# Kernel optimization log

Measured on AMD Instinct MI355X. Metric: run time of the kernel, lower is better.

## Reference

```python
import jax, jax.numpy as jnp
import numpy as np

B, LC, LQ, D = 256, 400, 50, 128
NEG = 1e12


def setup_inputs() -> dict:
    key = jax.random.key(0)
    ks = jax.random.split(key, 7)
    return {
        "x_cont": jax.random.normal(ks[0], (B, LC, D), dtype=jnp.float32),
        "x_ques": jax.random.normal(ks[1], (B, LQ, D), dtype=jnp.float32),
        "W0": jax.random.normal(ks[2], (D, 1), dtype=jnp.float32) * (1.0 / np.sqrt(D)),
        "W1": jax.random.normal(ks[3], (D, 1), dtype=jnp.float32) * (1.0 / np.sqrt(D)),
        "W2": jax.random.normal(ks[4], (1, 1, D), dtype=jnp.float32) * (1.0 / np.sqrt(D)),
        "cont_len": jax.random.randint(ks[5], (B, 1), 1, LC, dtype=jnp.int32),
        "ques_len": jax.random.randint(ks[6], (B, 1), 1, LQ, dtype=jnp.int32),
    }


def reference(x_cont, x_ques, W0, W1, W2, cont_len, ques_len):
    # Trilinear similarity S[b,c,q] = xc.W0 + xq.W1 + (xc*W2).xq
    s_c = x_cont @ W0                                   # (B, LC, 1)
    s_q = jnp.swapaxes(x_ques @ W1, 1, 2)               # (B, 1, LQ)
    s_f = jnp.einsum('bcd,bqd->bcq', x_cont * W2, x_ques)
    S = s_c + s_q + s_f                                 # (B, LC, LQ)

    # Length masks: position valid iff pos < seq_len (matches one_hot+cumsum)
    q_mask = (jnp.arange(LQ)[None, :] < ques_len).astype(S.dtype)  # (B, LQ)
    c_mask = (jnp.arange(LC)[None, :] < cont_len).astype(S.dtype)  # (B, LC)

    S_bar = jax.nn.softmax(S - (1.0 - q_mask)[:, None, :] * NEG, axis=-1)
    S_T = jnp.swapaxes(
        jax.nn.softmax(S - (1.0 - c_mask)[:, :, None] * NEG, axis=1), 1, 2)  # (B, LQ, LC)

    c2q = S_bar @ x_ques                                # (B, LC, D)
    q2c = (S_bar @ S_T) @ x_cont                        # (B, LC, D)

    result = jnp.concatenate(
        [x_cont, c2q, x_cont * c2q, x_cont * q2c], axis=-1)  # (B, LC, 4D)
    return result, S_bar, S_T
```

## Files before the change

### kernel.cpp

```cpp
#include <hip/hip_runtime.h>
#include <math.h>

#define B 256
#define LC 400
#define LQ 50
#define D 128
#define CT 64

__global__ __launch_bounds__(256, 2) void k_scores_rowsm(
    const float* __restrict__ xc_g, const float* __restrict__ xq_g,
    const float* __restrict__ W0, const float* __restrict__ W1,
    const float* __restrict__ W2, const int* __restrict__ ques_len,
    float* __restrict__ S_bar, float* __restrict__ S_Traw)
{
    __shared__ __align__(16) float xq[56 * 132];
    __shared__ __align__(16) float xc[CT * 132];
    __shared__ float w[3 * D];
    __shared__ float sq[56], sc[CT];
    __shared__ float sS[CT * 51];
    __shared__ float rowm[CT], rowi[CT];

    const int b = blockIdx.y;
    const int c0 = blockIdx.x * CT;
    const int t = threadIdx.x;
    const int nc = min(CT, LC - c0);
    const int qlen = ques_len[b];

    const float4* xq4g = (const float4*)(xq_g + (size_t)b * LQ * D);
    for (int i = t; i < 56 * 32; i += 256) {
        float4 v = (i < LQ * 32) ? xq4g[i] : make_float4(0.f, 0.f, 0.f, 0.f);
        ((float4*)xq)[(i >> 5) * 33 + (i & 31)] = v;
    }
    const float4* xc4g = (const float4*)(xc_g + (size_t)(b * LC + c0) * D);
    for (int i = t; i < nc * 32; i += 256)
        ((float4*)xc)[(i >> 5) * 33 + (i & 31)] = xc4g[i];
    if (t < D) { w[t] = W0[t]; w[D + t] = W1[t]; w[2 * D + t] = W2[t]; }
    __syncthreads();

    if (t < LQ) {
        const float4* r = (const float4*)(xq + t * 132);
        const float4* wv = (const float4*)(w + D);
        float4 a = {0.f, 0.f, 0.f, 0.f};
#pragma unroll
        for (int d = 0; d < 32; ++d) {
            float4 u = r[d], v = wv[d];
            a.x += u.x * v.x; a.y += u.y * v.y; a.z += u.z * v.z; a.w += u.w * v.w;
        }
        sq[t] = a.x + a.y + a.z + a.w;
    } else if (t >= 64 && t < 128) {
        const int c = t - 64;
        if (c < nc) {
            const float4* r = (const float4*)(xc + c * 132);
            const float4* wv = (const float4*)w;
            float4 a = {0.f, 0.f, 0.f, 0.f};
#pragma unroll
            for (int d = 0; d < 32; ++d) {
                float4 u = r[d], v = wv[d];
                a.x += u.x * v.x; a.y += u.y * v.y; a.z += u.z * v.z; a.w += u.w * v.w;
            }
            sc[c] = a.x + a.y + a.z + a.w;
        }
    }
    __syncthreads();
    for (int i = t; i < LQ * D; i += 256)
        xq[(i >> 7) * 132 + (i & 127)] *= w[2 * D + (i & 127)];
    __syncthreads();

    const int qg = t & 7;
    const int cg = (t >> 3) & 15;
    const int half = t >> 7;
    const int d0 = half * 16;

    float acc[4][7];
#pragma unroll
    for (int k = 0; k < 4; ++k)
#pragma unroll
        for (int j = 0; j < 7; ++j) acc[k][j] = 0.f;

    {
        const float4* xc4 = (const float4*)xc;
        const float4* xq4 = (const float4*)xq;
#pragma unroll 4
        for (int dd = 0; dd < 16; ++dd) {
            const int d4 = d0 + dd;
            const float4 a0 = xc4[(cg + 0)  * 33 + d4];
            const float4 a1 = xc4[(cg + 16) * 33 + d4];
            const float4 a2 = xc4[(cg + 32) * 33 + d4];
            const float4 a3 = xc4[(cg + 48) * 33 + d4];
#pragma unroll
            for (int j = 0; j < 7; ++j) {
                const float4 bq = xq4[(qg * 7 + j) * 33 + d4];
                acc[0][j] += a0.x*bq.x + a0.y*bq.y + a0.z*bq.z + a0.w*bq.w;
                acc[1][j] += a1.x*bq.x + a1.y*bq.y + a1.z*bq.z + a1.w*bq.w;
                acc[2][j] += a2.x*bq.x + a2.y*bq.y + a2.z*bq.z + a2.w*bq.w;
                acc[3][j] += a3.x*bq.x + a3.y*bq.y + a3.z*bq.z + a3.w*bq.w;
            }
        }
    }
    if (half) {
#pragma unroll
        for (int k = 0; k < 4; ++k) {
            const int c = cg + 16 * k;
            if (c < nc) {
#pragma unroll
                for (int j = 0; j < 7; ++j) {
                    const int q = qg * 7 + j;
                    if (q < LQ) sS[c * 51 + q] = acc[k][j];
                }
            }
        }
    }
    __syncthreads();
    if (!half) {
#pragma unroll
        for (int k = 0; k < 4; ++k) {
            const int c = cg + 16 * k;
            if (c < nc) {
                const float scc = sc[c];
#pragma unroll
                for (int j = 0; j < 7; ++j) {
                    const int q = qg * 7 + j;
                    if (q < LQ)
                        sS[c * 51 + q] = acc[k][j] + sS[c * 51 + q] + scc + sq[q];
                }
            }
        }
    }
    __syncthreads();

    if (t < nc) {
        float m = -INFINITY;
        for (int q = 0; q < qlen; ++q) m = fmaxf(m, sS[t * 51 + q]);
        float s = 0.f;
        for (int q = 0; q < qlen; ++q) s += __expf(sS[t * 51 + q] - m);
        rowm[t] = m;
        rowi[t] = 1.f / s;
    }
    __syncthreads();

    float* Sb = S_bar + (size_t)(b * LC + c0) * LQ;
    for (int i = t; i < nc * LQ; i += 256) {
        const int c = i / LQ, q = i - c * LQ;
        Sb[i] = (q < qlen) ? __expf(sS[c * 51 + q] - rowm[c]) * rowi[c] : 0.f;
    }
    float* STb = S_Traw + (size_t)b * LQ * LC + c0;
    for (int i = t; i < LQ * 64; i += 256) {
        const int q = i >> 6, c = i & 63;
        if (c < nc) STb[q * LC + c] = sS[c * 51 + q];
    }
}

__global__ __launch_bounds__(512) void k_colsm_qc(
    float* __restrict__ S_T, const float* __restrict__ xc_g,
    const int* __restrict__ cont_len, float* __restrict__ T)
{
    __shared__ __align__(16) float sT[56 * 404];
    __shared__ float red[256];
    __shared__ float colmax[LQ], colinv[LQ];

    const int b = blockIdx.x;
    const int t = threadIdx.x;
    const int clen = cont_len[b];
    float* STb = S_T + (size_t)b * LQ * LC;

    const float4* STb4 = (const float4*)STb;
    float4* sTw = (float4*)sT;
    for (int i = t; i < LQ * 100; i += 512)
        sTw[(i / 100) * 101 + (i % 100)] = STb4[i];
    __syncthreads();

    const int qr = t / 5, g = t - qr * 5;
    if (t < 250) {
        float m = -INFINITY;
        const int ce = min((g + 1) * 80, clen);
        for (int c = g * 80; c < ce; ++c) m = fmaxf(m, sT[qr * 404 + c]);
        red[t] = m;
    }
    __syncthreads();
    if (t < LQ) {
        float m = red[t * 5];
#pragma unroll
        for (int k = 1; k < 5; ++k) m = fmaxf(m, red[t * 5 + k]);
        colmax[t] = m;
    }
    __syncthreads();
    if (t < 250) {
        float s = 0.f;
        const float cm = colmax[qr];
        const int ce = min((g + 1) * 80, clen);
        for (int c = g * 80; c < ce; ++c) s += __expf(sT[qr * 404 + c] - cm);
        red[t] = s;
    }
    __syncthreads();
    if (t < LQ) {
        float s = red[t * 5];
#pragma unroll
        for (int k = 1; k < 5; ++k) s += red[t * 5 + k];
        colinv[t] = 1.f / s;
    }
    __syncthreads();

    for (int i = t; i < LQ * LC; i += 512) {
        const int q = i / LC, c = i - q * LC;
        const float v = (c < clen) ? __expf(sT[q * 404 + c] - colmax[q]) * colinv[q] : 0.f;
        sT[q * 404 + c] = v;
        STb[i] = v;
    }
    __syncthreads();

    const int d4 = t & 31, qg = t >> 5;
    const int qb = qg * 4;
    float4 acc[4];
#pragma unroll
    for (int j = 0; j < 4; ++j) acc[j] = make_float4(0.f, 0.f, 0.f, 0.f);

    const float4* xcv = (const float4*)xc_g + (size_t)b * LC * 32 + d4;
    const float4* sT4 = (const float4*)sT;
    for (int c = 0; c < LC; c += 4) {
        const float4 x0 = xcv[(c + 0) * 32];
        const float4 x1 = xcv[(c + 1) * 32];
        const float4 x2 = xcv[(c + 2) * 32];
        const float4 x3 = xcv[(c + 3) * 32];
#pragma unroll
        for (int j = 0; j < 4; ++j) {
            const int q = min(qb + j, LQ - 1);
            const float4 wv = sT4[q * 101 + (c >> 2)];
            acc[j].x += wv.x * x0.x + wv.y * x1.x + wv.z * x2.x + wv.w * x3.x;
            acc[j].y += wv.x * x0.y + wv.y * x1.y + wv.z * x2.y + wv.w * x3.y;
            acc[j].z += wv.x * x0.z + wv.y * x1.z + wv.z * x2.z + wv.w * x3.z;
            acc[j].w += wv.x * x0.w + wv.y * x1.w + wv.z * x2.w + wv.w * x3.w;
        }
    }
    float4* Tb = (float4*)T + (size_t)b * LQ * 32 + d4;
#pragma unroll
    for (int j = 0; j < 4; ++j) {
        const int q = qb + j;
        if (q < LQ) Tb[q * 32] = acc[j];
    }
}

#define FMA4(A, s, V) { A.x += (s) * V.x; A.y += (s) * V.y; A.z += (s) * V.z; A.w += (s) * V.w; }

__global__ __launch_bounds__(256, 2) void k_out(
    const float* __restrict__ S_bar, const float* __restrict__ xq_g,
    const float* __restrict__ Tm, const float* __restrict__ xc_g,
    float* __restrict__ out)
{
    __shared__ __align__(16) float xqL[LQ * 132];
    __shared__ __align__(16) float TL[LQ * 132];
    __shared__ __align__(16) float sbT[LQ * 68];

    const int b = blockIdx.y;
    const int c0 = blockIdx.x * CT;
    const int t = threadIdx.x;
    const int nc = min(CT, LC - c0);

    const float4* xq4g = (const float4*)(xq_g + (size_t)b * LQ * D);
    const float4* T4g  = (const float4*)(Tm + (size_t)b * LQ * D);
    for (int i = t; i < LQ * 32; i += 256) {
        const int row = i >> 5, col = i & 31;
        ((float4*)xqL)[row * 33 + col] = xq4g[i];
        ((float4*)TL)[row * 33 + col]  = T4g[i];
    }
    const float* sb_g = S_bar + (size_t)(b * LC + c0) * LQ;
    for (int i = t; i < CT * LQ; i += 256) {
        const int c = i / LQ, q = i - c * LQ;
        sbT[q * 68 + c] = (c < nc) ? sb_g[i] : 0.f;
    }

    const int d4 = t & 31, cg = t >> 5;
    const int cbase = cg * 8;

    const float4* xcv = (const float4*)xc_g;
    float4 xcr[8];
#pragma unroll
    for (int i = 0; i < 8; ++i) {
        int row = b * LC + c0 + cbase + i;
        row = min(row, B * LC - 1);
        xcr[i] = xcv[(size_t)row * 32 + d4];
    }
    __syncthreads();

    float4 c2q[8], q2c[8];
#pragma unroll
    for (int i = 0; i < 8; ++i) {
        c2q[i] = make_float4(0.f, 0.f, 0.f, 0.f);
        q2c[i] = make_float4(0.f, 0.f, 0.f, 0.f);
    }
    const float4* xq4 = (const float4*)xqL;
    const float4* T4  = (const float4*)TL;
    const float4* sb4 = (const float4*)sbT;
    const int cb2 = cg * 2;
    for (int qq = 0; qq < LQ; ++qq) {
        const float4 xv = xq4[qq * 33 + d4];
        const float4 tv = T4[qq * 33 + d4];
        const float4 s0 = sb4[qq * 17 + cb2];
        const float4 s1 = sb4[qq * 17 + cb2 + 1];
        FMA4(c2q[0], s0.x, xv); FMA4(q2c[0], s0.x, tv);
        FMA4(c2q[1], s0.y, xv); FMA4(q2c[1], s0.y, tv);
        FMA4(c2q[2], s0.z, xv); FMA4(q2c[2], s0.z, tv);
        FMA4(c2q[3], s0.w, xv); FMA4(q2c[3], s0.w, tv);
        FMA4(c2q[4], s1.x, xv); FMA4(q2c[4], s1.x, tv);
        FMA4(c2q[5], s1.y, xv); FMA4(q2c[5], s1.y, tv);
        FMA4(c2q[6], s1.z, xv); FMA4(q2c[6], s1.z, tv);
        FMA4(c2q[7], s1.w, xv); FMA4(q2c[7], s1.w, tv);
    }

    float4* out4 = (float4*)out;
#pragma unroll
    for (int i = 0; i < 8; ++i) {
        const int c = cbase + i;
        if (c < nc) {
            const int row = b * LC + c0 + c;
            const float4 xc = xcr[i];
            float4* o = out4 + (size_t)row * 128 + d4;
            o[0] = xc;
            o[32] = c2q[i];
            o[64] = make_float4(xc.x * c2q[i].x, xc.y * c2q[i].y,
                                xc.z * c2q[i].z, xc.w * c2q[i].w);
            o[96] = make_float4(xc.x * q2c[i].x, xc.y * q2c[i].y,
                                xc.z * q2c[i].z, xc.w * q2c[i].w);
        }
    }
}

extern "C" void kernel_launch(void* const* d_in, const int* in_sizes, int n_in,
                              void* d_out, int out_size, void* d_ws, size_t ws_size,
                              hipStream_t stream)
{
    (void)in_sizes; (void)n_in; (void)out_size; (void)ws_size;
    const float* x_cont = (const float*)d_in[0];
    const float* x_ques = (const float*)d_in[1];
    const float* W0 = (const float*)d_in[2];
    const float* W1 = (const float*)d_in[3];
    const float* W2 = (const float*)d_in[4];
    const int* cont_len = (const int*)d_in[5];
    const int* ques_len = (const int*)d_in[6];

    float* out = (float*)d_out;
    float* out_res  = out;
    float* out_Sbar = out + (size_t)B * LC * 4 * D;
    float* out_ST   = out_Sbar + (size_t)B * LC * LQ;
    float* Tws = (float*)d_ws;

    k_scores_rowsm<<<dim3(7, B), 256, 0, stream>>>(x_cont, x_ques, W0, W1, W2,
                                                   ques_len, out_Sbar, out_ST);
    k_colsm_qc<<<B, 512, 0, stream>>>(out_ST, x_cont, cont_len, Tws);
    k_out<<<dim3(7, B), 256, 0, stream>>>(out_Sbar, x_ques, Tws, x_cont, out_res);
}
```

Before: 439.8 us.

## Split column-softmax kernel across two query halves per batch

Splits the column-softmax and q-by-c product kernel into two blocks per batch, each handling 25 query rows. Shared memory use drops by roughly half, which allows more resident blocks per CU, doubles the grid to 512 blocks and widens the reduction to 16 segments per column. The cost is that each block now reads the full x_cont slice for its batch, so that global traffic doubles.

```diff
diff --git a/kernel.cpp b/kernel.cpp
--- a/kernel.cpp
+++ b/kernel.cpp
@@ -150,57 +150,59 @@
     }
 }
 
-__global__ __launch_bounds__(512) void k_colsm_qc(
+__global__ __launch_bounds__(512, 6) void k_colsm_qc(
     float* __restrict__ S_T, const float* __restrict__ xc_g,
     const int* __restrict__ cont_len, float* __restrict__ T)
 {
-    __shared__ __align__(16) float sT[56 * 404];
-    __shared__ float red[256];
-    __shared__ float colmax[LQ], colinv[LQ];
-
-    const int b = blockIdx.x;
+    __shared__ __align__(16) float sT[25 * 404];
+    __shared__ float red[400];
+    __shared__ float colmax[28], colinv[28];
+
+    const int half = blockIdx.x;
+    const int b = blockIdx.y;
+    const int q0 = half * 25;
     const int t = threadIdx.x;
     const int clen = cont_len[b];
-    float* STb = S_T + (size_t)b * LQ * LC;
+    float* STb = S_T + ((size_t)b * LQ + q0) * LC;
 
     const float4* STb4 = (const float4*)STb;
     float4* sTw = (float4*)sT;
-    for (int i = t; i < LQ * 100; i += 512)
+    for (int i = t; i < 25 * 100; i += 512)
         sTw[(i / 100) * 101 + (i % 100)] = STb4[i];
     __syncthreads();
 
-    const int qr = t / 5, g = t - qr * 5;
-    if (t < 250) {
+    const int qr = t >> 4, g = t & 15;
+    if (t < 400) {
+        const int cb = g * 25, ce = min(cb + 25, clen);
         float m = -INFINITY;
-        const int ce = min((g + 1) * 80, clen);
-        for (int c = g * 80; c < ce; ++c) m = fmaxf(m, sT[qr * 404 + c]);
+        for (int c = cb; c < ce; ++c) m = fmaxf(m, sT[qr * 404 + c]);
         red[t] = m;
     }
     __syncthreads();
-    if (t < LQ) {
-        float m = red[t * 5];
-#pragma unroll
-        for (int k = 1; k < 5; ++k) m = fmaxf(m, red[t * 5 + k]);
+    if (t < 25) {
+        float m = red[t * 16];
+#pragma unroll
+        for (int k = 1; k < 16; ++k) m = fmaxf(m, red[t * 16 + k]);
         colmax[t] = m;
     }
     __syncthreads();
-    if (t < 250) {
+    if (t < 400) {
+        const int cb = g * 25, ce = min(cb + 25, clen);
         float s = 0.f;
         const float cm = colmax[qr];
-        const int ce = min((g + 1) * 80, clen);
-        for (int c = g * 80; c < ce; ++c) s += __expf(sT[qr * 404 + c] - cm);
+        for (int c = cb; c < ce; ++c) s += __expf(sT[qr * 404 + c] - cm);
         red[t] = s;
     }
     __syncthreads();
-    if (t < LQ) {
-        float s = red[t * 5];
-#pragma unroll
-        for (int k = 1; k < 5; ++k) s += red[t * 5 + k];
+    if (t < 25) {
+        float s = red[t * 16];
+#pragma unroll
+        for (int k = 1; k < 16; ++k) s += red[t * 16 + k];
         colinv[t] = 1.f / s;
     }
     __syncthreads();
 
-    for (int i = t; i < LQ * LC; i += 512) {
+    for (int i = t; i < 25 * LC; i += 512) {
         const int q = i / LC, c = i - q * LC;
         const float v = (c < clen) ? __expf(sT[q * 404 + c] - colmax[q]) * colinv[q] : 0.f;
         sT[q * 404 + c] = v;
@@ -209,10 +211,9 @@
     __syncthreads();
 
     const int d4 = t & 31, qg = t >> 5;
-    const int qb = qg * 4;
-    float4 acc[4];
-#pragma unroll
-    for (int j = 0; j < 4; ++j) acc[j] = make_float4(0.f, 0.f, 0.f, 0.f);
+    float4 acc0 = make_float4(0.f, 0.f, 0.f, 0.f);
+    float4 acc1 = make_float4(0.f, 0.f, 0.f, 0.f);
+    const bool has1 = (qg + 16) < 25;
 
     const float4* xcv = (const float4*)xc_g + (size_t)b * LC * 32 + d4;
     const float4* sT4 = (const float4*)sT;
@@ -221,22 +222,24 @@
         const float4 x1 = xcv[(c + 1) * 32];
         const float4 x2 = xcv[(c + 2) * 32];
         const float4 x3 = xcv[(c + 3) * 32];
-#pragma unroll
-        for (int j = 0; j < 4; ++j) {
-            const int q = min(qb + j, LQ - 1);
-            const float4 wv = sT4[q * 101 + (c >> 2)];
-            acc[j].x += wv.x * x0.x + wv.y * x1.x + wv.z * x2.x + wv.w * x3.x;
-            acc[j].y += wv.x * x0.y + wv.y * x1.y + wv.z * x2.y + wv.w * x3.y;
-            acc[j].z += wv.x * x0.z + wv.y * x1.z + wv.z * x2.z + wv.w * x3.z;
-            acc[j].w += wv.x * x0.w + wv.y * x1.w + wv.z * x2.w + wv.w * x3.w;
+        {
+            const float4 wv = sT4[qg * 101 + (c >> 2)];
+            acc0.x += wv.x * x0.x + wv.y * x1.x + wv.z * x2.x + wv.w * x3.x;
+            acc0.y += wv.x * x0.y + wv.y * x1.y + wv.z * x2.y + wv.w * x3.y;
+            acc0.z += wv.x * x0.z + wv.y * x1.z + wv.z * x2.z + wv.w * x3.z;
+            acc0.w += wv.x * x0.w + wv.y * x1.w + wv.z * x2.w + wv.w * x3.w;
+        }
+        if (has1) {
+            const float4 wv = sT4[(qg + 16) * 101 + (c >> 2)];
+            acc1.x += wv.x * x0.x + wv.y * x1.x + wv.z * x2.x + wv.w * x3.x;
+            acc1.y += wv.x * x0.y + wv.y * x1.y + wv.z * x2.y + wv.w * x3.y;
+            acc1.z += wv.x * x0.z + wv.y * x1.z + wv.z * x2.z + wv.w * x3.z;
+            acc1.w += wv.x * x0.w + wv.y * x1.w + wv.z * x2.w + wv.w * x3.w;
         }
     }
     float4* Tb = (float4*)T + (size_t)b * LQ * 32 + d4;
-#pragma unroll
-    for (int j = 0; j < 4; ++j) {
-        const int q = qb + j;
-        if (q < LQ) Tb[q * 32] = acc[j];
-    }
+    Tb[(q0 + qg) * 32] = acc0;
+    if (has1) Tb[(q0 + qg + 16) * 32] = acc1;
 }
 
 #define FMA4(A, s, V) { A.x += (s) * V.x; A.y += (s) * V.y; A.z += (s) * V.z; A.w += (s) * V.w; }
@@ -345,6 +348,6 @@
 
     k_scores_rowsm<<<dim3(7, B), 256, 0, stream>>>(x_cont, x_ques, W0, W1, W2,
                                                    ques_len, out_Sbar, out_ST);
-    k_colsm_qc<<<B, 512, 0, stream>>>(out_ST, x_cont, cont_len, Tws);
+    k_colsm_qc<<<dim3(2, B), 512, 0, stream>>>(out_ST, x_cont, cont_len, Tws);
     k_out<<<dim3(7, B), 256, 0, stream>>>(out_Sbar, x_ques, Tws, x_cont, out_res);
 }
```

After: 456.3 us. 1.04x slower.
